# Optimization experiments

Measured on AMD Instinct MI355X. Metric: run time of the kernel, lower is better.

## Reference

```python
import jax, jax.numpy as jnp
import numpy as np

N = 50000      # n_nodes
E = 800000     # n_edges (avg degree 16)
IN, HID, OUT = 64, 128, 64


def setup_inputs() -> dict:
    key = jax.random.key(0)
    ks = jax.random.split(key, 7)
    x = jax.random.normal(ks[0], (N, IN), dtype=jnp.float32)
    src = jax.random.randint(ks[1], (E,), 0, N, dtype=jnp.int64)
    dst = jax.random.randint(ks[2], (E,), 0, N, dtype=jnp.int64)
    # Glorot-uniform init like DGL GraphConv
    lim1 = np.sqrt(6.0 / (IN + HID))
    lim2 = np.sqrt(6.0 / (HID + OUT))
    W1 = jax.random.uniform(ks[3], (IN, HID), jnp.float32, -lim1, lim1)
    b1 = jnp.zeros((HID,), jnp.float32)
    W2 = jax.random.uniform(ks[4], (HID, OUT), jnp.float32, -lim2, lim2)
    b2 = jnp.zeros((OUT,), jnp.float32)
    return {"x": x, "W1": W1, "b1": b1, "W2": W2, "b2": b2, "src": src, "dst": dst}


def _graph_conv(x, W, b, src, dst, norm_src, norm_dst):
    """DGL GraphConv with norm='both': D_in^{-1/2} A D_out^{-1/2} x W + b.
    Applies W before aggregation iff in_feats > out_feats (as DGL does),
    so the edge gather always happens on the narrower feature width."""
    in_f, out_f = W.shape
    h = x * norm_src[:, None]                      # [N, in_f]
    if in_f > out_f:
        h = h @ W                                   # [N, out_f]
        m = jax.ops.segment_sum(h[src], dst, num_segments=N)  # [N, out_f]
    else:
        m = jax.ops.segment_sum(h[src], dst, num_segments=N) @ W
    return m * norm_dst[:, None] + b


def reference(x, W1, b1, W2, b2, src, dst):
    ones = jnp.ones((E,), x.dtype)
    out_deg = jax.ops.segment_sum(ones, src, num_segments=N)
    in_deg = jax.ops.segment_sum(ones, dst, num_segments=N)
    norm_src = jnp.clip(out_deg, 1.0, None) ** -0.5  # clamp(min=1) like DGL
    norm_dst = jnp.clip(in_deg, 1.0, None) ** -0.5
    h = jax.nn.relu(_graph_conv(x, W1, b1, src, dst, norm_src, norm_dst))
    return _graph_conv(h, W2, b2, src, dst, norm_src, norm_dst)
```

## Files before the change

### kernel.cpp

```cpp
#include <hip/hip_runtime.h>

#define N_NODES 50000
#define N_EDGES 800000
#define SCAN_BLOCKS ((N_NODES + 255) / 256)
#define CHUNKS 64
#define EDGES_PER_CHUNK (N_EDGES / CHUNKS)
#define QUARTER_NODES 12500
#define WORDS_PER_QUARTER 6250
#define REP_WORDS 25000

typedef unsigned short ushort_t;
typedef __attribute__((ext_vector_type(8))) short bf16x8;
typedef __attribute__((ext_vector_type(4))) float f32x4;

static __device__ __forceinline__ ushort_t f2bf(float f) {
    unsigned u = __float_as_uint(f);
    unsigned r = (u + 0x7fffu + ((u >> 16) & 1u)) >> 16;
    return (ushort_t)r;
}
static __device__ __forceinline__ float bf2f(ushort_t u) {
    return __uint_as_float(((unsigned)u) << 16);
}

__global__ __launch_bounds__(1024) void hist_kernel(const int* __restrict__ src,
                                                    const int* __restrict__ dst,
                                                    unsigned int* __restrict__ rep) {
    __shared__ unsigned int cnt[WORDS_PER_QUARTER];
    int bid = blockIdx.x;
    int chunk = bid & 63;
    int qf = (bid >> 6) & 3;
    int arr = bid >> 8;
    const int* ids = arr ? dst : src;
    int tid = threadIdx.x;
    for (int i = tid; i < WORDS_PER_QUARTER; i += 1024) cnt[i] = 0;
    __syncthreads();
    int base = qf * QUARTER_NODES;
    int ebeg = chunk * EDGES_PER_CHUNK;
    for (int i = tid; i < EDGES_PER_CHUNK; i += 1024) {
        int v = ids[ebeg + i] - base;
        if ((unsigned)v < (unsigned)QUARTER_NODES)
            atomicAdd(&cnt[v >> 1], 1u << ((v & 1) << 4));
    }
    __syncthreads();
    unsigned int* o = rep + ((size_t)arr * CHUNKS + chunk) * REP_WORDS + qf * WORDS_PER_QUARTER;
    for (int i = tid; i < WORDS_PER_QUARTER; i += 1024) o[i] = cnt[i];
}

__global__ __launch_bounds__(256) void scan1_kernel(const unsigned int* __restrict__ rep,
                                                    int* __restrict__ indeg,
                                                    int* __restrict__ tmp_incl,
                                                    int* __restrict__ bsum) {
    __shared__ int lds[256];
    int tid = threadIdx.x;
    int i = blockIdx.x * 256 + tid;
    int v = 0;
    if (i < N_NODES) {
        int w = i >> 1, sh = (i & 1) << 4;
        const unsigned int* repd = rep + (size_t)CHUNKS * REP_WORDS;
        #pragma unroll 8
        for (int c = 0; c < CHUNKS; c++)
            v += (int)((repd[(size_t)c * REP_WORDS + w] >> sh) & 0xffffu);
        indeg[i] = v;
    }
    lds[tid] = v;
    __syncthreads();
    for (int off = 1; off < 256; off <<= 1) {
        int t = (tid >= off) ? lds[tid - off] : 0;
        __syncthreads();
        lds[tid] += t;
        __syncthreads();
    }
    if (i < N_NODES) tmp_incl[i] = lds[tid];
    if (tid == 255) bsum[blockIdx.x] = lds[255];
}

__global__ __launch_bounds__(256) void scan2_kernel(const int* __restrict__ bsum,
                                                    int* __restrict__ bofs,
                                                    int* __restrict__ row_start) {
    __shared__ int lds[256];
    int tid = threadIdx.x;
    lds[tid] = (tid < SCAN_BLOCKS) ? bsum[tid] : 0;
    __syncthreads();
    for (int off = 1; off < 256; off <<= 1) {
        int t = (tid >= off) ? lds[tid - off] : 0;
        __syncthreads();
        lds[tid] += t;
        __syncthreads();
    }
    if (tid < SCAN_BLOCKS) bofs[tid] = (tid == 0) ? 0 : lds[tid - 1];
    if (tid == SCAN_BLOCKS - 1) row_start[N_NODES] = lds[tid];
}

__global__ __launch_bounds__(256) void scan3_kernel(const unsigned int* __restrict__ rep,
                                                    const int* __restrict__ indeg,
                                                    const int* __restrict__ tmp_incl,
                                                    const int* __restrict__ bofs,
                                                    const float* __restrict__ x,
                                                    int* __restrict__ row_start,
                                                    float* __restrict__ norm_src,
                                                    float* __restrict__ norm_dst,
                                                    int* __restrict__ cbase,
                                                    ushort_t* __restrict__ xs) {
    int i = blockIdx.x * 256 + threadIdx.x;
    if (i >= N_NODES) return;
    int id = indeg[i];
    int rs = bofs[blockIdx.x] + tmp_incl[i] - id;
    row_start[i] = rs;
    int w = i >> 1, sh = (i & 1) << 4;
    int od = 0;
    #pragma unroll 8
    for (int c = 0; c < CHUNKS; c++)
        od += (int)((rep[(size_t)c * REP_WORDS + w] >> sh) & 0xffffu);
    float ns = 1.0f / sqrtf((float)max(od, 1));
    norm_src[i] = ns;
    norm_dst[i] = 1.0f / sqrtf((float)max(id, 1));
    const unsigned int* repd = rep + (size_t)CHUNKS * REP_WORDS;
    int running = rs;
    for (int c = 0; c < CHUNKS; c++) {
        cbase[(size_t)c * N_NODES + i] = running;
        running += (int)((repd[(size_t)c * REP_WORDS + w] >> sh) & 0xffffu);
    }
    #pragma unroll
    for (int q = 0; q < 16; q++) {
        float4 v = *(const float4*)&x[(size_t)i * 64 + q * 4];
        ushort_t* o = &xs[(size_t)i * 64 + q * 4];
        o[0] = f2bf(v.x * ns); o[1] = f2bf(v.y * ns);
        o[2] = f2bf(v.z * ns); o[3] = f2bf(v.w * ns);
    }
}

__global__ __launch_bounds__(1024) void fill2_kernel(const int* __restrict__ src,
                                                     const int* __restrict__ dst,
                                                     const int* __restrict__ cbase,
                                                     int* __restrict__ edge_src) {
    __shared__ unsigned int rank[WORDS_PER_QUARTER];
    int chunk = blockIdx.x & 63;
    int qf = blockIdx.x >> 6;
    int tid = threadIdx.x;
    for (int i = tid; i < WORDS_PER_QUARTER; i += 1024) rank[i] = 0;
    __syncthreads();
    int base = qf * QUARTER_NODES;
    int ebeg = chunk * EDGES_PER_CHUNK;
    for (int i = tid; i < EDGES_PER_CHUNK; i += 1024) {
        int d = dst[ebeg + i];
        int v = d - base;
        if ((unsigned)v < (unsigned)QUARTER_NODES) {
            int sh = (v & 1) << 4;
            unsigned old = atomicAdd(&rank[v >> 1], 1u << sh);
            int r = (int)((old >> sh) & 0xffffu);
            int pos = cbase[(size_t)chunk * N_NODES + d] + r;
            edge_src[pos] = src[ebeg + i];
        }
    }
}

__global__ __launch_bounds__(256) void gather1_kernel(
        const ushort_t* __restrict__ xs, const int* __restrict__ edge_src,
        const int* __restrict__ row_start, float* __restrict__ agg) {
    int node = (blockIdx.x * blockDim.x + threadIdx.x) >> 6;
    int lane = threadIdx.x & 63;
    int grp = lane >> 4;
    int lpos = lane & 15;
    int beg = row_start[node];
    int end = row_start[node + 1];
    float a0 = 0.f, a1 = 0.f, a2 = 0.f, a3 = 0.f;
    for (int i = beg; i < end; i += 64) {
        int cnt = min(end - i, 64);
        int ids = (lane < cnt) ? edge_src[i + lane] : 0;
        for (int t = 0; t < cnt; t += 16) {
            #pragma unroll
            for (int q = 0; q < 4; q++) {
                int j = t + 4 * q + grp;
                int jj = max(min(j, cnt - 1), 0);
                int s = __builtin_amdgcn_ds_bpermute(jj << 2, ids);
                uint2 v = *(const uint2*)&xs[(size_t)s * 64 + lpos * 4];
                float m = (j < cnt) ? 1.f : 0.f;
                a0 = fmaf(__uint_as_float(v.x << 16), m, a0);
                a1 = fmaf(__uint_as_float(v.x & 0xffff0000u), m, a1);
                a2 = fmaf(__uint_as_float(v.y << 16), m, a2);
                a3 = fmaf(__uint_as_float(v.y & 0xffff0000u), m, a3);
            }
        }
    }
    a0 += __shfl_xor(a0, 16, 64); a1 += __shfl_xor(a1, 16, 64);
    a2 += __shfl_xor(a2, 16, 64); a3 += __shfl_xor(a3, 16, 64);
    a0 += __shfl_xor(a0, 32, 64); a1 += __shfl_xor(a1, 32, 64);
    a2 += __shfl_xor(a2, 32, 64); a3 += __shfl_xor(a3, 32, 64);
    if (grp == 0)
        *(float4*)&agg[(size_t)node * 64 + lpos * 4] = make_float4(a0, a1, a2, a3);
}

__global__ __launch_bounds__(256) void gather2_kernel(
        const ushort_t* __restrict__ h2, const int* __restrict__ edge_src,
        const int* __restrict__ row_start, const float* __restrict__ norm_dst,
        const float* __restrict__ b2, float* __restrict__ out) {
    int node = (blockIdx.x * blockDim.x + threadIdx.x) >> 6;
    int lane = threadIdx.x & 63;
    int grp = lane >> 4;
    int lpos = lane & 15;
    int beg = row_start[node];
    int end = row_start[node + 1];
    float a0 = 0.f, a1 = 0.f, a2 = 0.f, a3 = 0.f;
    for (int i = beg; i < end; i += 64) {
        int cnt = min(end - i, 64);
        int ids = (lane < cnt) ? edge_src[i + lane] : 0;
        for (int t = 0; t < cnt; t += 16) {
            #pragma unroll
            for (int q = 0; q < 4; q++) {
                int j = t + 4 * q + grp;
                int jj = max(min(j, cnt - 1), 0);
                int s = __builtin_amdgcn_ds_bpermute(jj << 2, ids);
                uint2 v = *(const uint2*)&h2[(size_t)s * 64 + lpos * 4];
                float m = (j < cnt) ? 1.f : 0.f;
                a0 = fmaf(__uint_as_float(v.x << 16), m, a0);
                a1 = fmaf(__uint_as_float(v.x & 0xffff0000u), m, a1);
                a2 = fmaf(__uint_as_float(v.y << 16), m, a2);
                a3 = fmaf(__uint_as_float(v.y & 0xffff0000u), m, a3);
            }
        }
    }
    a0 += __shfl_xor(a0, 16, 64); a1 += __shfl_xor(a1, 16, 64);
    a2 += __shfl_xor(a2, 16, 64); a3 += __shfl_xor(a3, 16, 64);
    a0 += __shfl_xor(a0, 32, 64); a1 += __shfl_xor(a1, 32, 64);
    a2 += __shfl_xor(a2, 32, 64); a3 += __shfl_xor(a3, 32, 64);
    if (grp == 0) {
        float nd = norm_dst[node];
        float4 bb = *(const float4*)&b2[lpos * 4];
        *(float4*)&out[(size_t)node * 64 + lpos * 4] =
            make_float4(a0 * nd + bb.x, a1 * nd + bb.y, a2 * nd + bb.z, a3 * nd + bb.w);
    }
}

__global__ __launch_bounds__(256) void gemm_fused_kernel(
        const float* __restrict__ agg, const float* __restrict__ W1,
        const float* __restrict__ b1, const float* __restrict__ W2,
        const float* __restrict__ norm_dst, const float* __restrict__ norm_src,
        ushort_t* __restrict__ h2) {
    __shared__ ushort_t mem[18432];
    ushort_t* As_hi = mem;
    ushort_t* As_lo = mem + 4608;
    ushort_t* Wt1   = mem + 9216;
    int tid = threadIdx.x;
    int rowbase = blockIdx.x * 64;

    for (int i = tid; i < 8192; i += 256) {
        int k = i >> 7, n = i & 127;
        Wt1[n * 72 + k] = f2bf(W1[i]);
    }
    for (int i = tid; i < 1024; i += 256) {
        int row = i >> 4;
        int c = (i & 15) * 4;
        int gr = rowbase + row;
        float4 v = make_float4(0.f, 0.f, 0.f, 0.f);
        if (gr < N_NODES) v = *(const float4*)&agg[(size_t)gr * 64 + c];
        float va[4] = {v.x, v.y, v.z, v.w};
        int base = row * 72 + c;
        #pragma unroll
        for (int q = 0; q < 4; q++) {
            ushort_t h = f2bf(va[q]);
            As_hi[base + q] = h;
            As_lo[base + q] = f2bf(va[q] - bf2f(h));
        }
    }
    __syncthreads();

    int lane = tid & 63;
    int w = tid >> 6;
    int lr = lane & 15;
    int hi8 = lane >> 4;
    int a_off = (16 * w + lr) * 72 + hi8 * 8;

    f32x4 acc[8] = {};
    #pragma unroll
    for (int ks = 0; ks < 2; ks++) {
        bf16x8 ah = *(bf16x8*)&As_hi[a_off + ks * 32];
        bf16x8 al = *(bf16x8*)&As_lo[a_off + ks * 32];
        #pragma unroll
        for (int ct = 0; ct < 8; ct++) {
            bf16x8 b = *(bf16x8*)&Wt1[(ct * 16 + lr) * 72 + ks * 32 + hi8 * 8];
            acc[ct] = __builtin_amdgcn_mfma_f32_16x16x32_bf16(ah, b, acc[ct], 0, 0, 0);
            acc[ct] = __builtin_amdgcn_mfma_f32_16x16x32_bf16(al, b, acc[ct], 0, 0, 0);
        }
    }

    int row4 = hi8 * 4;
    float nd[4], ns[4];
    #pragma unroll
    for (int r = 0; r < 4; r++) {
        int gr = rowbase + 16 * w + row4 + r;
        nd[r] = (gr < N_NODES) ? norm_dst[gr] : 0.f;
        ns[r] = (gr < N_NODES) ? norm_src[gr] : 0.f;
    }
    __syncthreads();

    ushort_t* Hs  = mem;
    ushort_t* Wt2 = mem + 8704;
    for (int i = tid; i < 8192; i += 256) {
        int k = i >> 6, n = i & 63;
        Wt2[n * 136 + k] = f2bf(W2[i]);
    }
    #pragma unroll
    for (int ct = 0; ct < 8; ct++) {
        float bb = b1[ct * 16 + lr];
        #pragma unroll
        for (int r = 0; r < 4; r++) {
            float v = fmaxf(acc[ct][r] * nd[r] + bb, 0.f) * ns[r];
            Hs[(16 * w + row4 + r) * 136 + ct * 16 + lr] = f2bf(v);
        }
    }
    __syncthreads();

    f32x4 acc2[4] = {};
    int a2_off = (16 * w + lr) * 136 + hi8 * 8;
    #pragma unroll
    for (int ks = 0; ks < 4; ks++) {
        bf16x8 a2 = *(bf16x8*)&Hs[a2_off + ks * 32];
        #pragma unroll
        for (int ct = 0; ct < 4; ct++) {
            bf16x8 b = *(bf16x8*)&Wt2[(ct * 16 + lr) * 136 + ks * 32 + hi8 * 8];
            acc2[ct] = __builtin_amdgcn_mfma_f32_16x16x32_bf16(a2, b, acc2[ct], 0, 0, 0);
        }
    }
    #pragma unroll
    for (int ct = 0; ct < 4; ct++) {
        #pragma unroll
        for (int r = 0; r < 4; r++) {
            int gr = rowbase + 16 * w + row4 + r;
            if (gr < N_NODES)
                h2[(size_t)gr * 64 + ct * 16 + lr] = f2bf(acc2[ct][r]);
        }
    }
}

extern "C" void kernel_launch(void* const* d_in, const int* in_sizes, int n_in,
                              void* d_out, int out_size, void* d_ws, size_t ws_size,
                              hipStream_t stream) {
    const float* x  = (const float*)d_in[0];
    const float* W1 = (const float*)d_in[1];
    const float* b1 = (const float*)d_in[2];
    const float* W2 = (const float*)d_in[3];
    const float* b2 = (const float*)d_in[4];
    const int* src  = (const int*)d_in[5];
    const int* dst  = (const int*)d_in[6];
    float* out = (float*)d_out;

    int* indeg = (int*)d_ws;
    float* norm_src = (float*)(indeg + N_NODES);
    float* norm_dst = norm_src + N_NODES;
    int* row_start = (int*)(norm_dst + N_NODES);
    int* tmp_incl = row_start + N_NODES + 1;
    int* bsum = tmp_incl + N_NODES;
    int* bofs = bsum + SCAN_BLOCKS;
    unsigned int* rep = (unsigned int*)(bofs + SCAN_BLOCKS);
    int* edge_src = (int*)(rep + (size_t)2 * CHUNKS * REP_WORDS);
    int* cbase = edge_src + N_EDGES;
    float* agg1 = (float*)cbase;
    ushort_t* xs = (ushort_t*)(agg1 + (size_t)N_NODES * 64);
    ushort_t* h2 = xs + (size_t)N_NODES * 64;

    hist_kernel<<<512, 1024, 0, stream>>>(src, dst, rep);
    scan1_kernel<<<SCAN_BLOCKS, 256, 0, stream>>>(rep, indeg, tmp_incl, bsum);
    scan2_kernel<<<1, 256, 0, stream>>>(bsum, bofs, row_start);
    scan3_kernel<<<SCAN_BLOCKS, 256, 0, stream>>>(rep, indeg, tmp_incl, bofs, x,
                                                  row_start, norm_src, norm_dst,
                                                  cbase, xs);
    fill2_kernel<<<256, 1024, 0, stream>>>(src, dst, cbase, edge_src);
    gather1_kernel<<<(N_NODES * 64) / 256, 256, 0, stream>>>(
        xs, edge_src, row_start, agg1);
    gemm_fused_kernel<<<(N_NODES + 63) / 64, 256, 0, stream>>>(
        agg1, W1, b1, W2, norm_dst, norm_src, h2);
    gather2_kernel<<<(N_NODES * 64) / 256, 256, 0, stream>>>(
        h2, edge_src, row_start, norm_dst, b2, out);
}
```

Before: 103.8 us.

## Widen gather loads to 16 bytes and precompute bf16 transposed weights once

The gather kernels now have each lane load 8 bf16 values (16 bytes) per neighbor row, so 8 edges are processed concurrently per wave and fewer load instructions are issued. A new small kernel converts and transposes W1/W2 to padded bf16 once in workspace. Each gemm block then copies those words into shared memory instead of redoing the conversion. This adds one kernel launch and more accumulator registers in the gathers.

```diff
diff --git a/kernel.cpp b/kernel.cpp
--- a/kernel.cpp
+++ b/kernel.cpp
@@ -44,6 +44,21 @@
     __syncthreads();
     unsigned int* o = rep + ((size_t)arr * CHUNKS + chunk) * REP_WORDS + qf * WORDS_PER_QUARTER;
     for (int i = tid; i < WORDS_PER_QUARTER; i += 1024) o[i] = cnt[i];
+}
+
+__global__ __launch_bounds__(256) void wconv_kernel(const float* __restrict__ W1,
+                                                    const float* __restrict__ W2,
+                                                    ushort_t* __restrict__ wt1g,
+                                                    ushort_t* __restrict__ wt2g) {
+    int i = blockIdx.x * 256 + threadIdx.x;
+    if (i < 8192) {
+        int k = i >> 7, n = i & 127;
+        wt1g[n * 72 + k] = f2bf(W1[i]);
+    } else {
+        int j = i - 8192;
+        int k = j >> 6, n = j & 63;
+        wt2g[n * 136 + k] = f2bf(W2[j]);
+    }
 }
 
 __global__ __launch_bounds__(256) void scan1_kernel(const unsigned int* __restrict__ rep,
@@ -159,35 +174,45 @@
         const int* __restrict__ row_start, float* __restrict__ agg) {
     int node = (blockIdx.x * blockDim.x + threadIdx.x) >> 6;
     int lane = threadIdx.x & 63;
-    int grp = lane >> 4;
-    int lpos = lane & 15;
+    int grp = lane >> 3;
+    int lpos = lane & 7;
     int beg = row_start[node];
     int end = row_start[node + 1];
     float a0 = 0.f, a1 = 0.f, a2 = 0.f, a3 = 0.f;
+    float a4 = 0.f, a5 = 0.f, a6 = 0.f, a7 = 0.f;
     for (int i = beg; i < end; i += 64) {
         int cnt = min(end - i, 64);
         int ids = (lane < cnt) ? edge_src[i + lane] : 0;
         for (int t = 0; t < cnt; t += 16) {
             #pragma unroll
-            for (int q = 0; q < 4; q++) {
-                int j = t + 4 * q + grp;
+            for (int q = 0; q < 2; q++) {
+                int j = t + 8 * q + grp;
                 int jj = max(min(j, cnt - 1), 0);
                 int s = __builtin_amdgcn_ds_bpermute(jj << 2, ids);
-                uint2 v = *(const uint2*)&xs[(size_t)s * 64 + lpos * 4];
+                uint4 v = *(const uint4*)&xs[(size_t)s * 64 + lpos * 8];
                 float m = (j < cnt) ? 1.f : 0.f;
                 a0 = fmaf(__uint_as_float(v.x << 16), m, a0);
                 a1 = fmaf(__uint_as_float(v.x & 0xffff0000u), m, a1);
                 a2 = fmaf(__uint_as_float(v.y << 16), m, a2);
                 a3 = fmaf(__uint_as_float(v.y & 0xffff0000u), m, a3);
+                a4 = fmaf(__uint_as_float(v.z << 16), m, a4);
+                a5 = fmaf(__uint_as_float(v.z & 0xffff0000u), m, a5);
+                a6 = fmaf(__uint_as_float(v.w << 16), m, a6);
+                a7 = fmaf(__uint_as_float(v.w & 0xffff0000u), m, a7);
             }
         }
     }
-    a0 += __shfl_xor(a0, 16, 64); a1 += __shfl_xor(a1, 16, 64);
-    a2 += __shfl_xor(a2, 16, 64); a3 += __shfl_xor(a3, 16, 64);
-    a0 += __shfl_xor(a0, 32, 64); a1 += __shfl_xor(a1, 32, 64);
-    a2 += __shfl_xor(a2, 32, 64); a3 += __shfl_xor(a3, 32, 64);
-    if (grp == 0)
-        *(float4*)&agg[(size_t)node * 64 + lpos * 4] = make_float4(a0, a1, a2, a3);
+    #pragma unroll
+    for (int off = 8; off <= 32; off <<= 1) {
+        a0 += __shfl_xor(a0, off, 64); a1 += __shfl_xor(a1, off, 64);
+        a2 += __shfl_xor(a2, off, 64); a3 += __shfl_xor(a3, off, 64);
+        a4 += __shfl_xor(a4, off, 64); a5 += __shfl_xor(a5, off, 64);
+        a6 += __shfl_xor(a6, off, 64); a7 += __shfl_xor(a7, off, 64);
+    }
+    if (grp == 0) {
+        *(float4*)&agg[(size_t)node * 64 + lpos * 8] = make_float4(a0, a1, a2, a3);
+        *(float4*)&agg[(size_t)node * 64 + lpos * 8 + 4] = make_float4(a4, a5, a6, a7);
+    }
 }
 
 __global__ __launch_bounds__(256) void gather2_kernel(
@@ -196,44 +221,55 @@
         const float* __restrict__ b2, float* __restrict__ out) {
     int node = (blockIdx.x * blockDim.x + threadIdx.x) >> 6;
     int lane = threadIdx.x & 63;
-    int grp = lane >> 4;
-    int lpos = lane & 15;
+    int grp = lane >> 3;
+    int lpos = lane & 7;
     int beg = row_start[node];
     int end = row_start[node + 1];
     float a0 = 0.f, a1 = 0.f, a2 = 0.f, a3 = 0.f;
+    float a4 = 0.f, a5 = 0.f, a6 = 0.f, a7 = 0.f;
     for (int i = beg; i < end; i += 64) {
         int cnt = min(end - i, 64);
         int ids = (lane < cnt) ? edge_src[i + lane] : 0;
         for (int t = 0; t < cnt; t += 16) {
             #pragma unroll
-            for (int q = 0; q < 4; q++) {
-                int j = t + 4 * q + grp;
+            for (int q = 0; q < 2; q++) {
+                int j = t + 8 * q + grp;
                 int jj = max(min(j, cnt - 1), 0);
                 int s = __builtin_amdgcn_ds_bpermute(jj << 2, ids);
-                uint2 v = *(const uint2*)&h2[(size_t)s * 64 + lpos * 4];
+                uint4 v = *(const uint4*)&h2[(size_t)s * 64 + lpos * 8];
                 float m = (j < cnt) ? 1.f : 0.f;
                 a0 = fmaf(__uint_as_float(v.x << 16), m, a0);
                 a1 = fmaf(__uint_as_float(v.x & 0xffff0000u), m, a1);
                 a2 = fmaf(__uint_as_float(v.y << 16), m, a2);
                 a3 = fmaf(__uint_as_float(v.y & 0xffff0000u), m, a3);
+                a4 = fmaf(__uint_as_float(v.z << 16), m, a4);
+                a5 = fmaf(__uint_as_float(v.z & 0xffff0000u), m, a5);
+                a6 = fmaf(__uint_as_float(v.w << 16), m, a6);
+                a7 = fmaf(__uint_as_float(v.w & 0xffff0000u), m, a7);
             }
         }
     }
-    a0 += __shfl_xor(a0, 16, 64); a1 += __shfl_xor(a1, 16, 64);
-    a2 += __shfl_xor(a2, 16, 64); a3 += __shfl_xor(a3, 16, 64);
-    a0 += __shfl_xor(a0, 32, 64); a1 += __shfl_xor(a1, 32, 64);
-    a2 += __shfl_xor(a2, 32, 64); a3 += __shfl_xor(a3, 32, 64);
+    #pragma unroll
+    for (int off = 8; off <= 32; off <<= 1) {
+        a0 += __shfl_xor(a0, off, 64); a1 += __shfl_xor(a1, off, 64);
+        a2 += __shfl_xor(a2, off, 64); a3 += __shfl_xor(a3, off, 64);
+        a4 += __shfl_xor(a4, off, 64); a5 += __shfl_xor(a5, off, 64);
+        a6 += __shfl_xor(a6, off, 64); a7 += __shfl_xor(a7, off, 64);
+    }
     if (grp == 0) {
         float nd = norm_dst[node];
-        float4 bb = *(const float4*)&b2[lpos * 4];
-        *(float4*)&out[(size_t)node * 64 + lpos * 4] =
-            make_float4(a0 * nd + bb.x, a1 * nd + bb.y, a2 * nd + bb.z, a3 * nd + bb.w);
+        float4 b_lo = *(const float4*)&b2[lpos * 8];
+        float4 b_hi = *(const float4*)&b2[lpos * 8 + 4];
+        *(float4*)&out[(size_t)node * 64 + lpos * 8] =
+            make_float4(a0 * nd + b_lo.x, a1 * nd + b_lo.y, a2 * nd + b_lo.z, a3 * nd + b_lo.w);
+        *(float4*)&out[(size_t)node * 64 + lpos * 8 + 4] =
+            make_float4(a4 * nd + b_hi.x, a5 * nd + b_hi.y, a6 * nd + b_hi.z, a7 * nd + b_hi.w);
     }
 }
 
 __global__ __launch_bounds__(256) void gemm_fused_kernel(
-        const float* __restrict__ agg, const float* __restrict__ W1,
-        const float* __restrict__ b1, const float* __restrict__ W2,
+        const float* __restrict__ agg, const ushort_t* __restrict__ wt1g,
+        const float* __restrict__ b1, const ushort_t* __restrict__ wt2g,
         const float* __restrict__ norm_dst, const float* __restrict__ norm_src,
         ushort_t* __restrict__ h2) {
     __shared__ ushort_t mem[18432];
@@ -243,10 +279,8 @@
     int tid = threadIdx.x;
     int rowbase = blockIdx.x * 64;
 
-    for (int i = tid; i < 8192; i += 256) {
-        int k = i >> 7, n = i & 127;
-        Wt1[n * 72 + k] = f2bf(W1[i]);
-    }
+    for (int i = tid; i < 4608; i += 256)
+        ((unsigned*)Wt1)[i] = ((const unsigned*)wt1g)[i];
     for (int i = tid; i < 1024; i += 256) {
         int row = i >> 4;
         int c = (i & 15) * 4;
@@ -295,10 +329,8 @@
 
     ushort_t* Hs  = mem;
     ushort_t* Wt2 = mem + 8704;
-    for (int i = tid; i < 8192; i += 256) {
-        int k = i >> 6, n = i & 63;
-        Wt2[n * 136 + k] = f2bf(W2[i]);
-    }
+    for (int i = tid; i < 4352; i += 256)
+        ((unsigned*)Wt2)[i] = ((const unsigned*)wt2g)[i];
     #pragma unroll
     for (int ct = 0; ct < 8; ct++) {
         float bb = b1[ct * 16 + lr];
@@ -351,7 +383,9 @@
     int* tmp_incl = row_start + N_NODES + 1;
     int* bsum = tmp_incl + N_NODES;
     int* bofs = bsum + SCAN_BLOCKS;
-    unsigned int* rep = (unsigned int*)(bofs + SCAN_BLOCKS);
+    ushort_t* wt1g = (ushort_t*)(bofs + SCAN_BLOCKS);
+    ushort_t* wt2g = wt1g + 9216;
+    unsigned int* rep = (unsigned int*)(wt2g + 8704 + 16);
     int* edge_src = (int*)(rep + (size_t)2 * CHUNKS * REP_WORDS);
     int* cbase = edge_src + N_EDGES;
     float* agg1 = (float*)cbase;
@@ -359,6 +393,7 @@
     ushort_t* h2 = xs + (size_t)N_NODES * 64;
 
     hist_kernel<<<512, 1024, 0, stream>>>(src, dst, rep);
+    wconv_kernel<<<64, 256, 0, stream>>>(W1, W2, wt1g, wt2g);
     scan1_kernel<<<SCAN_BLOCKS, 256, 0, stream>>>(rep, indeg, tmp_incl, bsum);
     scan2_kernel<<<1, 256, 0, stream>>>(bsum, bofs, row_start);
     scan3_kernel<<<SCAN_BLOCKS, 256, 0, stream>>>(rep, indeg, tmp_incl, bofs, x,
@@ -368,7 +403,7 @@
     gather1_kernel<<<(N_NODES * 64) / 256, 256, 0, stream>>>(
         xs, edge_src, row_start, agg1);
     gemm_fused_kernel<<<(N_NODES + 63) / 64, 256, 0, stream>>>(
-        agg1, W1, b1, W2, norm_dst, norm_src, h2);
+        agg1, wt1g, b1, wt2g, norm_dst, norm_src, h2);
     gather2_kernel<<<(N_NODES * 64) / 256, 256, 0, stream>>>(
         h2, edge_src, row_start, norm_dst, b2, out);
 }
```

After: 105.1 us. About the same (+1.2%).

## Fuse layer-1 gather into fused GEMM kernel and pre-convert weights once

Applied to the files above, without the earlier changes.

Merges the first edge-gather kernel into the fused two-layer GEMM kernel. Each block now aggregates its 64 nodes directly into LDS as hi/lo bf16 splits, so the fp32 agg buffer is no longer written to and read back from global memory. Weight transpose and bf16 conversion move into a small separate kernel that runs once, and the GEMM reads B fragments from global or L2 instead of rebuilding them in LDS in every block. The cost is less gather parallelism per block: each wave walks 16 nodes in sequence, and only 782 blocks of 4 waves run, which may hurt latency hiding for the irregular gathers.

```diff
diff --git a/kernel.cpp b/kernel.cpp
--- a/kernel.cpp
+++ b/kernel.cpp
@@ -44,6 +44,21 @@
     __syncthreads();
     unsigned int* o = rep + ((size_t)arr * CHUNKS + chunk) * REP_WORDS + qf * WORDS_PER_QUARTER;
     for (int i = tid; i < WORDS_PER_QUARTER; i += 1024) o[i] = cnt[i];
+}
+
+__global__ __launch_bounds__(256) void wconv_kernel(const float* __restrict__ W1,
+                                                    const float* __restrict__ W2,
+                                                    ushort_t* __restrict__ wt1g,
+                                                    ushort_t* __restrict__ wt2g) {
+    int i = blockIdx.x * 256 + threadIdx.x;
+    if (i < 8192) {
+        int k = i >> 7, n = i & 127;
+        wt1g[n * 72 + k] = f2bf(W1[i]);
+    } else {
+        int j = i - 8192;
+        int k = j >> 6, n = j & 63;
+        wt2g[n * 136 + k] = f2bf(W2[j]);
+    }
 }
 
 __global__ __launch_bounds__(256) void scan1_kernel(const unsigned int* __restrict__ rep,
@@ -154,40 +169,123 @@
     }
 }
 
-__global__ __launch_bounds__(256) void gather1_kernel(
+__global__ __launch_bounds__(256) void gemm_fused_kernel(
         const ushort_t* __restrict__ xs, const int* __restrict__ edge_src,
-        const int* __restrict__ row_start, float* __restrict__ agg) {
-    int node = (blockIdx.x * blockDim.x + threadIdx.x) >> 6;
-    int lane = threadIdx.x & 63;
+        const int* __restrict__ row_start, const ushort_t* __restrict__ wt1g,
+        const float* __restrict__ b1, const ushort_t* __restrict__ wt2g,
+        const float* __restrict__ norm_dst, const float* __restrict__ norm_src,
+        ushort_t* __restrict__ h2) {
+    __shared__ ushort_t mem[9216];
+    ushort_t* As_hi = mem;
+    ushort_t* As_lo = mem + 4608;
+    int tid = threadIdx.x;
+    int w = tid >> 6;
+    int lane = tid & 63;
     int grp = lane >> 4;
     int lpos = lane & 15;
-    int beg = row_start[node];
-    int end = row_start[node + 1];
-    float a0 = 0.f, a1 = 0.f, a2 = 0.f, a3 = 0.f;
-    for (int i = beg; i < end; i += 64) {
-        int cnt = min(end - i, 64);
-        int ids = (lane < cnt) ? edge_src[i + lane] : 0;
-        for (int t = 0; t < cnt; t += 16) {
-            #pragma unroll
-            for (int q = 0; q < 4; q++) {
-                int j = t + 4 * q + grp;
-                int jj = max(min(j, cnt - 1), 0);
-                int s = __builtin_amdgcn_ds_bpermute(jj << 2, ids);
-                uint2 v = *(const uint2*)&xs[(size_t)s * 64 + lpos * 4];
-                float m = (j < cnt) ? 1.f : 0.f;
-                a0 = fmaf(__uint_as_float(v.x << 16), m, a0);
-                a1 = fmaf(__uint_as_float(v.x & 0xffff0000u), m, a1);
-                a2 = fmaf(__uint_as_float(v.y << 16), m, a2);
-                a3 = fmaf(__uint_as_float(v.y & 0xffff0000u), m, a3);
+    int rowbase = blockIdx.x * 64;
+
+    for (int k = 0; k < 16; k++) {
+        int nl = w * 16 + k;
+        int node = rowbase + nl;
+        float a0 = 0.f, a1 = 0.f, a2 = 0.f, a3 = 0.f;
+        if (node < N_NODES) {
+            int beg = row_start[node];
+            int end = row_start[node + 1];
+            for (int i = beg; i < end; i += 64) {
+                int cnt = min(end - i, 64);
+                int ids = (lane < cnt) ? edge_src[i + lane] : 0;
+                for (int t = 0; t < cnt; t += 16) {
+                    #pragma unroll
+                    for (int q = 0; q < 4; q++) {
+                        int j = t + 4 * q + grp;
+                        int jj = max(min(j, cnt - 1), 0);
+                        int s = __builtin_amdgcn_ds_bpermute(jj << 2, ids);
+                        uint2 v = *(const uint2*)&xs[(size_t)s * 64 + lpos * 4];
+                        float m = (j < cnt) ? 1.f : 0.f;
+                        a0 = fmaf(__uint_as_float(v.x << 16), m, a0);
+                        a1 = fmaf(__uint_as_float(v.x & 0xffff0000u), m, a1);
+                        a2 = fmaf(__uint_as_float(v.y << 16), m, a2);
+                        a3 = fmaf(__uint_as_float(v.y & 0xffff0000u), m, a3);
+                    }
+                }
             }
-        }
-    }
-    a0 += __shfl_xor(a0, 16, 64); a1 += __shfl_xor(a1, 16, 64);
-    a2 += __shfl_xor(a2, 16, 64); a3 += __shfl_xor(a3, 16, 64);
-    a0 += __shfl_xor(a0, 32, 64); a1 += __shfl_xor(a1, 32, 64);
-    a2 += __shfl_xor(a2, 32, 64); a3 += __shfl_xor(a3, 32, 64);
-    if (grp == 0)
-        *(float4*)&agg[(size_t)node * 64 + lpos * 4] = make_float4(a0, a1, a2, a3);
+            a0 += __shfl_xor(a0, 16, 64); a1 += __shfl_xor(a1, 16, 64);
+            a2 += __shfl_xor(a2, 16, 64); a3 += __shfl_xor(a3, 16, 64);
+            a0 += __shfl_xor(a0, 32, 64); a1 += __shfl_xor(a1, 32, 64);
+            a2 += __shfl_xor(a2, 32, 64); a3 += __shfl_xor(a3, 32, 64);
+        }
+        if (grp == 0) {
+            ushort_t h0 = f2bf(a0), h1 = f2bf(a1), h2v = f2bf(a2), h3 = f2bf(a3);
+            ushort_t l0 = f2bf(a0 - bf2f(h0)), l1 = f2bf(a1 - bf2f(h1));
+            ushort_t l2 = f2bf(a2 - bf2f(h2v)), l3 = f2bf(a3 - bf2f(h3));
+            int off = nl * 72 + lpos * 4;
+            *(uint2*)&As_hi[off] = make_uint2((unsigned)h0 | ((unsigned)h1 << 16),
+                                              (unsigned)h2v | ((unsigned)h3 << 16));
+            *(uint2*)&As_lo[off] = make_uint2((unsigned)l0 | ((unsigned)l1 << 16),
+                                              (unsigned)l2 | ((unsigned)l3 << 16));
+        }
+    }
+    __syncthreads();
+
+    int lr = lane & 15;
+    int hi8 = lane >> 4;
+    int a_off = (16 * w + lr) * 72 + hi8 * 8;
+    f32x4 acc[8] = {};
+    #pragma unroll
+    for (int ks = 0; ks < 2; ks++) {
+        bf16x8 ah = *(bf16x8*)&As_hi[a_off + ks * 32];
+        bf16x8 al = *(bf16x8*)&As_lo[a_off + ks * 32];
+        #pragma unroll
+        for (int ct = 0; ct < 8; ct++) {
+            bf16x8 b = *(const bf16x8*)&wt1g[(ct * 16 + lr) * 72 + ks * 32 + hi8 * 8];
+            acc[ct] = __builtin_amdgcn_mfma_f32_16x16x32_bf16(ah, b, acc[ct], 0, 0, 0);
+            acc[ct] = __builtin_amdgcn_mfma_f32_16x16x32_bf16(al, b, acc[ct], 0, 0, 0);
+        }
+    }
+
+    int row4 = hi8 * 4;
+    float nd[4], ns[4];
+    #pragma unroll
+    for (int r = 0; r < 4; r++) {
+        int gr = rowbase + 16 * w + row4 + r;
+        nd[r] = (gr < N_NODES) ? norm_dst[gr] : 0.f;
+        ns[r] = (gr < N_NODES) ? norm_src[gr] : 0.f;
+    }
+    __syncthreads();
+
+    ushort_t* Hs = mem;
+    #pragma unroll
+    for (int ct = 0; ct < 8; ct++) {
+        float bb = b1[ct * 16 + lr];
+        #pragma unroll
+        for (int r = 0; r < 4; r++) {
+            float v = fmaxf(acc[ct][r] * nd[r] + bb, 0.f) * ns[r];
+            Hs[(16 * w + row4 + r) * 136 + ct * 16 + lr] = f2bf(v);
+        }
+    }
+    __syncthreads();
+
+    f32x4 acc2[4] = {};
+    int a2_off = (16 * w + lr) * 136 + hi8 * 8;
+    #pragma unroll
+    for (int ks = 0; ks < 4; ks++) {
+        bf16x8 a2 = *(bf16x8*)&Hs[a2_off + ks * 32];
+        #pragma unroll
+        for (int ct = 0; ct < 4; ct++) {
+            bf16x8 b = *(const bf16x8*)&wt2g[(ct * 16 + lr) * 136 + ks * 32 + hi8 * 8];
+            acc2[ct] = __builtin_amdgcn_mfma_f32_16x16x32_bf16(a2, b, acc2[ct], 0, 0, 0);
+        }
+    }
+    #pragma unroll
+    for (int ct = 0; ct < 4; ct++) {
+        #pragma unroll
+        for (int r = 0; r < 4; r++) {
+            int gr = rowbase + 16 * w + row4 + r;
+            if (gr < N_NODES)
+                h2[(size_t)gr * 64 + ct * 16 + lr] = f2bf(acc2[ct][r]);
+        }
+    }
 }
 
 __global__ __launch_bounds__(256) void gather2_kernel(
@@ -231,107 +329,6 @@
     }
 }
 
-__global__ __launch_bounds__(256) void gemm_fused_kernel(
-        const float* __restrict__ agg, const float* __restrict__ W1,
-        const float* __restrict__ b1, const float* __restrict__ W2,
-        const float* __restrict__ norm_dst, const float* __restrict__ norm_src,
-        ushort_t* __restrict__ h2) {
-    __shared__ ushort_t mem[18432];
-    ushort_t* As_hi = mem;
-    ushort_t* As_lo = mem + 4608;
-    ushort_t* Wt1   = mem + 9216;
-    int tid = threadIdx.x;
-    int rowbase = blockIdx.x * 64;
-
-    for (int i = tid; i < 8192; i += 256) {
-        int k = i >> 7, n = i & 127;
-        Wt1[n * 72 + k] = f2bf(W1[i]);
-    }
-    for (int i = tid; i < 1024; i += 256) {
-        int row = i >> 4;
-        int c = (i & 15) * 4;
-        int gr = rowbase + row;
-        float4 v = make_float4(0.f, 0.f, 0.f, 0.f);
-        if (gr < N_NODES) v = *(const float4*)&agg[(size_t)gr * 64 + c];
-        float va[4] = {v.x, v.y, v.z, v.w};
-        int base = row * 72 + c;
-        #pragma unroll
-        for (int q = 0; q < 4; q++) {
-            ushort_t h = f2bf(va[q]);
-            As_hi[base + q] = h;
-            As_lo[base + q] = f2bf(va[q] - bf2f(h));
-        }
-    }
-    __syncthreads();
-
-    int lane = tid & 63;
-    int w = tid >> 6;
-    int lr = lane & 15;
-    int hi8 = lane >> 4;
-    int a_off = (16 * w + lr) * 72 + hi8 * 8;
-
-    f32x4 acc[8] = {};
-    #pragma unroll
-    for (int ks = 0; ks < 2; ks++) {
-        bf16x8 ah = *(bf16x8*)&As_hi[a_off + ks * 32];
-        bf16x8 al = *(bf16x8*)&As_lo[a_off + ks * 32];
-        #pragma unroll
-        for (int ct = 0; ct < 8; ct++) {
-            bf16x8 b = *(bf16x8*)&Wt1[(ct * 16 + lr) * 72 + ks * 32 + hi8 * 8];
-            acc[ct] = __builtin_amdgcn_mfma_f32_16x16x32_bf16(ah, b, acc[ct], 0, 0, 0);
-            acc[ct] = __builtin_amdgcn_mfma_f32_16x16x32_bf16(al, b, acc[ct], 0, 0, 0);
-        }
-    }
-
-    int row4 = hi8 * 4;
-    float nd[4], ns[4];
-    #pragma unroll
-    for (int r = 0; r < 4; r++) {
-        int gr = rowbase + 16 * w + row4 + r;
-        nd[r] = (gr < N_NODES) ? norm_dst[gr] : 0.f;
-        ns[r] = (gr < N_NODES) ? norm_src[gr] : 0.f;
-    }
-    __syncthreads();
-
-    ushort_t* Hs  = mem;
-    ushort_t* Wt2 = mem + 8704;
-    for (int i = tid; i < 8192; i += 256) {
-        int k = i >> 6, n = i & 63;
-        Wt2[n * 136 + k] = f2bf(W2[i]);
-    }
-    #pragma unroll
-    for (int ct = 0; ct < 8; ct++) {
-        float bb = b1[ct * 16 + lr];
-        #pragma unroll
-        for (int r = 0; r < 4; r++) {
-            float v = fmaxf(acc[ct][r] * nd[r] + bb, 0.f) * ns[r];
-            Hs[(16 * w + row4 + r) * 136 + ct * 16 + lr] = f2bf(v);
-        }
-    }
-    __syncthreads();
-
-    f32x4 acc2[4] = {};
-    int a2_off = (16 * w + lr) * 136 + hi8 * 8;
-    #pragma unroll
-    for (int ks = 0; ks < 4; ks++) {
-        bf16x8 a2 = *(bf16x8*)&Hs[a2_off + ks * 32];
-        #pragma unroll
-        for (int ct = 0; ct < 4; ct++) {
-            bf16x8 b = *(bf16x8*)&Wt2[(ct * 16 + lr) * 136 + ks * 32 + hi8 * 8];
-            acc2[ct] = __builtin_amdgcn_mfma_f32_16x16x32_bf16(a2, b, acc2[ct], 0, 0, 0);
-        }
-    }
-    #pragma unroll
-    for (int ct = 0; ct < 4; ct++) {
-        #pragma unroll
-        for (int r = 0; r < 4; r++) {
-            int gr = rowbase + 16 * w + row4 + r;
-            if (gr < N_NODES)
-                h2[(size_t)gr * 64 + ct * 16 + lr] = f2bf(acc2[ct][r]);
-        }
-    }
-}
-
 extern "C" void kernel_launch(void* const* d_in, const int* in_sizes, int n_in,
                               void* d_out, int out_size, void* d_ws, size_t ws_size,
                               hipStream_t stream) {
@@ -351,24 +348,24 @@
     int* tmp_incl = row_start + N_NODES + 1;
     int* bsum = tmp_incl + N_NODES;
     int* bofs = bsum + SCAN_BLOCKS;
-    unsigned int* rep = (unsigned int*)(bofs + SCAN_BLOCKS);
+    ushort_t* wt1g = (ushort_t*)(bofs + SCAN_BLOCKS);
+    ushort_t* wt2g = wt1g + 9216;
+    unsigned int* rep = (unsigned int*)(wt2g + 8704 + 16);
     int* edge_src = (int*)(rep + (size_t)2 * CHUNKS * REP_WORDS);
     int* cbase = edge_src + N_EDGES;
-    float* agg1 = (float*)cbase;
-    ushort_t* xs = (ushort_t*)(agg1 + (size_t)N_NODES * 64);
+    ushort_t* xs = (ushort_t*)(cbase + (size_t)CHUNKS * N_NODES);
     ushort_t* h2 = xs + (size_t)N_NODES * 64;
 
     hist_kernel<<<512, 1024, 0, stream>>>(src, dst, rep);
+    wconv_kernel<<<64, 256, 0, stream>>>(W1, W2, wt1g, wt2g);
     scan1_kernel<<<SCAN_BLOCKS, 256, 0, stream>>>(rep, indeg, tmp_incl, bsum);
     scan2_kernel<<<1, 256, 0, stream>>>(bsum, bofs, row_start);
     scan3_kernel<<<SCAN_BLOCKS, 256, 0, stream>>>(rep, indeg, tmp_incl, bofs, x,
                                                   row_start, norm_src, norm_dst,
                                                   cbase, xs);
     fill2_kernel<<<256, 1024, 0, stream>>>(src, dst, cbase, edge_src);
-    gather1_kernel<<<(N_NODES * 64) / 256, 256, 0, stream>>>(
-        xs, edge_src, row_start, agg1);
     gemm_fused_kernel<<<(N_NODES + 63) / 64, 256, 0, stream>>>(
-        agg1, W1, b1, W2, norm_dst, norm_src, h2);
+        xs, edge_src, row_start, wt1g, b1, wt2g, norm_dst, norm_src, h2);
     gather2_kernel<<<(N_NODES * 64) / 256, 256, 0, stream>>>(
         h2, edge_src, row_start, norm_dst, b2, out);
 }
```

Result: slower. 113.8 us (+9.6%).
